# Performance work log

Hardware: AMD Instinct MI355X
Metric: run time of the kernel (lower is better)

The kernel has to match this reference:

```python
import jax, jax.numpy as jnp
import numpy as np

N = 50000
E = 800000
D_IN = 128
D_H = 128
N_CLASSES = 40
N_HIDDEN = 2


def _gcn_norm(edge_index, num_nodes):
    # Add self loops, compute symmetric normalization D^-1/2 (A+I) D^-1/2
    loops = jnp.arange(num_nodes, dtype=edge_index.dtype)
    src = jnp.concatenate([edge_index[0], loops])
    dst = jnp.concatenate([edge_index[1], loops])
    deg = jax.ops.segment_sum(jnp.ones_like(src, dtype=jnp.float32), dst,
                              num_segments=num_nodes)
    dinv = jnp.where(deg > 0, jax.lax.rsqrt(jnp.maximum(deg, 1.0)), 0.0)
    norm = dinv[src] * dinv[dst]  # [E+N]
    return src, dst, norm


def _gcn_conv(x, src, dst, norm, W, b):
    h = x @ W                          # [N, d_out] transform first (PyG order)
    msg = h[src] * norm[:, None]       # gather + scale, [E+N, d_out]
    out = jax.ops.segment_sum(msg, dst, num_segments=x.shape[0])
    return out + b


def setup_inputs() -> dict:
    key = jax.random.key(0)
    ks = jax.random.split(key, 8)
    x = jax.random.normal(ks[0], (N, D_IN), dtype=jnp.float32)
    edge_index = jax.random.randint(ks[1], (2, E), 0, N, dtype=jnp.int64)
    s = 1.0 / np.sqrt(D_IN)
    W1 = jax.random.uniform(ks[2], (D_IN, D_H), minval=-s, maxval=s, dtype=jnp.float32)
    b1 = jnp.zeros((D_H,), dtype=jnp.float32)
    sh = 1.0 / np.sqrt(D_H)
    Wh = jax.random.uniform(ks[3], (N_HIDDEN, D_H, D_H), minval=-sh, maxval=sh, dtype=jnp.float32)
    bh = jnp.zeros((N_HIDDEN, D_H), dtype=jnp.float32)
    Wf = jax.random.uniform(ks[4], (D_H, N_CLASSES), minval=-sh, maxval=sh, dtype=jnp.float32)
    bf = jnp.zeros((N_CLASSES,), dtype=jnp.float32)
    return {"x": x, "edge_index": edge_index, "W1": W1, "b1": b1,
            "Wh": Wh, "bh": bh, "Wf": Wf, "bf": bf}


def reference(x, edge_index, W1, b1, Wh, bh, Wf, bf):
    src, dst, norm = _gcn_norm(edge_index, x.shape[0])
    h = jax.nn.relu(_gcn_conv(x, src, dst, norm, W1, b1))
    for i in range(Wh.shape[0]):  # small fixed layer count
        h = jax.nn.relu(_gcn_conv(h, src, dst, norm, Wh[i], bh[i]))
    # extra relu in original forward is a no-op after relu above
    return h @ Wf + bf
```

## Files before the change

### kernel.cpp

```cpp
#include <hip/hip_runtime.h>

#define D 128
#define NC 40

typedef __attribute__((ext_vector_type(8))) short short8v;
typedef __attribute__((ext_vector_type(4))) float f32x4;

__device__ __forceinline__ unsigned short f2bf(float f) {
    unsigned u = __float_as_uint(f);
    u += 0x7fff + ((u >> 16) & 1);
    return (unsigned short)(u >> 16);
}
__device__ __forceinline__ float bf2f(unsigned short h) {
    return __uint_as_float(((unsigned)h) << 16);
}


__global__ void detect_kernel(const int* __restrict__ ei, int* __restrict__ flag) {
    __shared__ int any;
    if (threadIdx.x == 0) any = 0;
    __syncthreads();
    if (ei[threadIdx.x * 2 + 1] != 0) any = 1;
    __syncthreads();
    if (threadIdx.x == 0) *flag = (any == 0) ? 1 : 0;
}

__device__ __forceinline__ int load_idx(const int* ei, long long pos, int is64) {
    return is64 ? ei[pos * 2] : ei[pos];
}

__global__ void count_deg_kernel(const int* __restrict__ ei, const int* __restrict__ flag,
                                 int* __restrict__ deg, int E) {
    int e = blockIdx.x * blockDim.x + threadIdx.x;
    if (e >= E) return;
    int is64 = *flag;
    int d = load_idx(ei, (long long)E + e, is64);
    atomicAdd(&deg[d], 1);
}

__global__ void scan1_kernel(const int* __restrict__ deg, int* __restrict__ bsum, int n) {
    int i = blockIdx.x * 256 + threadIdx.x;
    int v = (i < n) ? deg[i] : 0;
    #pragma unroll
    for (int off = 32; off; off >>= 1) v += __shfl_down(v, off, 64);
    __shared__ int ws[4];
    if ((threadIdx.x & 63) == 0) ws[threadIdx.x >> 6] = v;
    __syncthreads();
    if (threadIdx.x == 0) bsum[blockIdx.x] = ws[0] + ws[1] + ws[2] + ws[3];
}

__global__ void scan2_kernel(int* __restrict__ bsum, int* __restrict__ total, int nb) {
    int t = threadIdx.x;
    int lane = t & 63, w = t >> 6;
    int v = (t < nb) ? bsum[t] : 0;
    int s = v;
    #pragma unroll
    for (int off = 1; off < 64; off <<= 1) {
        int x = __shfl_up(s, off, 64);
        if (lane >= off) s += x;
    }
    __shared__ int wsum[16];
    if (lane == 63) wsum[w] = s;
    __syncthreads();
    int wbase = 0;
    #pragma unroll
    for (int j = 0; j < 16; ++j) if (j < w) wbase += wsum[j];
    int excl = wbase + s - v;
    if (t < nb) bsum[t] = excl;
    if (t == nb - 1) *total = excl + v;
}

__global__ void scan3_kernel(const int* __restrict__ deg, const int* __restrict__ bsum,
                             const int* __restrict__ total, int* __restrict__ rowptr,
                             int* __restrict__ fill, float* __restrict__ dinv, int n) {
    int i = blockIdx.x * 256 + threadIdx.x;
    int v = (i < n) ? deg[i] : 0;
    int lane = threadIdx.x & 63, w = threadIdx.x >> 6;
    int s = v;
    #pragma unroll
    for (int off = 1; off < 64; off <<= 1) {
        int x = __shfl_up(s, off, 64);
        if (lane >= off) s += x;
    }
    __shared__ int wsum[4];
    if (lane == 63) wsum[w] = s;
    __syncthreads();
    int wbase = 0;
    #pragma unroll
    for (int j = 0; j < 4; ++j) if (j < w) wbase += wsum[j];
    int excl = bsum[blockIdx.x] + wbase + s - v;
    if (i < n) {
        rowptr[i] = excl;
        fill[i]   = excl;
        dinv[i]   = rsqrtf((float)(v + 1));
    }
    if (i == 0) rowptr[n] = *total;
}

__global__ void scatter_kernel(const int* __restrict__ ei, const int* __restrict__ flag,
                               int* __restrict__ fill, const float* __restrict__ dinv,
                               int2* __restrict__ col2, int E) {
    int e = blockIdx.x * blockDim.x + threadIdx.x;
    if (e >= E) return;
    int is64 = *flag;
    int s = load_idx(ei, (long long)e, is64);
    int d = load_idx(ei, (long long)E + e, is64);
    int pos = atomicAdd(&fill[d], 1);
    col2[pos] = make_int2(s, __float_as_int(dinv[s]));
}

__global__ void convertW_kernel(const float* __restrict__ W, unsigned short* __restrict__ hi,
                                unsigned short* __restrict__ lo, int N, int Npad) {
    int idx = blockIdx.x * blockDim.x + threadIdx.x;
    if (idx >= Npad * 128) return;
    int nn = idx >> 7, k = idx & 127;
    float v = (nn < N) ? W[k * N + nn] : 0.f;
    unsigned short h = f2bf(v);
    hi[idx] = h;
    lo[idx] = f2bf(v - bf2f(h));
}

__launch_bounds__(256)
__global__ void gemm128_mfma_kernel(const float* __restrict__ A, const unsigned short* __restrict__ Wcvt,
                                    float* __restrict__ C, int M) {
    __shared__ unsigned short Ah[64 * 128];
    __shared__ unsigned short Al[64 * 128];
    int t = threadIdx.x;
    int l = t & 63, w = t >> 6;
    int lr = l & 15, lh = l >> 4;

    const unsigned short* Whi = Wcvt;
    const unsigned short* Wlo = Wcvt + 128 * 128;
    short8v bhi[2][4], blo[2][4];
    int n0 = w * 32;
    #pragma unroll
    for (int ni = 0; ni < 2; ++ni) {
        int n = n0 + ni * 16 + lr;
        #pragma unroll
        for (int ks = 0; ks < 4; ++ks) {
            bhi[ni][ks] = *(const short8v*)&Whi[n * 128 + ks * 32 + lh * 8];
            blo[ni][ks] = *(const short8v*)&Wlo[n * 128 + ks * 32 + lh * 8];
        }
    }

    int row0 = blockIdx.x * 64;
    #pragma unroll
    for (int c = 0; c < 4; ++c) {
        int chunk = c * 256 + t;
        int r  = chunk >> 4;
        int kc = chunk & 15;
        int gr = row0 + r; if (gr >= M) gr = M - 1;
        float4 a0 = *(const float4*)&A[(size_t)gr * 128 + kc * 8];
        float4 a1 = *(const float4*)&A[(size_t)gr * 128 + kc * 8 + 4];
        float av[8] = {a0.x, a0.y, a0.z, a0.w, a1.x, a1.y, a1.z, a1.w};
        short8v hv, lv;
        #pragma unroll
        for (int j = 0; j < 8; ++j) {
            unsigned short hi = f2bf(av[j]);
            hv[j] = (short)hi;
            lv[j] = (short)f2bf(av[j] - bf2f(hi));
        }
        int off = (r << 8) + ((kc << 4) ^ ((r & 7) << 4));
        *(short8v*)((char*)Ah + off) = hv;
        *(short8v*)((char*)Al + off) = lv;
    }
    __syncthreads();

    f32x4 acc[4][2];
    #pragma unroll
    for (int mi = 0; mi < 4; ++mi)
        #pragma unroll
        for (int ni = 0; ni < 2; ++ni)
            acc[mi][ni] = (f32x4){0.f, 0.f, 0.f, 0.f};

    #pragma unroll
    for (int mi = 0; mi < 4; ++mi) {
        int row = mi * 16 + lr;
        #pragma unroll
        for (int ks = 0; ks < 4; ++ks) {
            int off = (row << 8) + (((ks << 6) + (lh << 4)) ^ ((row & 7) << 4));
            short8v ah = *(short8v*)((char*)Ah + off);
            short8v al = *(short8v*)((char*)Al + off);
            #pragma unroll
            for (int ni = 0; ni < 2; ++ni) {
                acc[mi][ni] = __builtin_amdgcn_mfma_f32_16x16x32_bf16(ah, bhi[ni][ks], acc[mi][ni], 0, 0, 0);
                acc[mi][ni] = __builtin_amdgcn_mfma_f32_16x16x32_bf16(ah, blo[ni][ks], acc[mi][ni], 0, 0, 0);
                acc[mi][ni] = __builtin_amdgcn_mfma_f32_16x16x32_bf16(al, bhi[ni][ks], acc[mi][ni], 0, 0, 0);
            }
        }
    }

    #pragma unroll
    for (int mi = 0; mi < 4; ++mi) {
        #pragma unroll
        for (int ni = 0; ni < 2; ++ni) {
            #pragma unroll
            for (int r = 0; r < 4; ++r) {
                int row = row0 + mi * 16 + lh * 4 + r;
                if (row < M) C[(size_t)row * 128 + n0 + ni * 16 + lr] = acc[mi][ni][r];
            }
        }
    }
}

__launch_bounds__(256)
__global__ void aggregate_kernel(const float4* __restrict__ h4, const float* __restrict__ dinv,
                                 const int* __restrict__ rowptr, const int2* __restrict__ col2,
                                 const float* __restrict__ bias, float4* __restrict__ out4, int n) {
    int node = blockIdx.x * 8 + (threadIdx.x >> 5);
    if (node >= n) return;
    int l = threadIdx.x & 31;
    float dn = dinv[node];
    size_t rowbase = (size_t)node * 32;
    float4 hv = h4[rowbase + l];
    float4 acc;
    acc.x = hv.x * dn; acc.y = hv.y * dn; acc.z = hv.z * dn; acc.w = hv.w * dn;
    int e = rowptr[node], e1 = rowptr[node + 1];
    int2 c[8];
    #pragma unroll
    for (int j = 0; j < 8; ++j)
        c[j] = (e + j < e1) ? col2[e + j] : make_int2(node, 0);
    while (e < e1) {
        int en = e + 8;
        int2 cn[8];
        #pragma unroll
        for (int j = 0; j < 8; ++j)
            cn[j] = (en + j < e1) ? col2[en + j] : make_int2(node, 0);
        float4 v[8];
        #pragma unroll
        for (int j = 0; j < 8; ++j) v[j] = h4[(size_t)c[j].x * 32 + l];
        #pragma unroll
        for (int j = 0; j < 8; ++j) {
            float ds = __int_as_float(c[j].y);
            acc.x += v[j].x * ds; acc.y += v[j].y * ds;
            acc.z += v[j].z * ds; acc.w += v[j].w * ds;
        }
        #pragma unroll
        for (int j = 0; j < 8; ++j) c[j] = cn[j];
        e = en;
    }
    float4 bv = *(const float4*)&bias[l * 4];
    float4 o;
    o.x = fmaxf(acc.x * dn + bv.x, 0.f);
    o.y = fmaxf(acc.y * dn + bv.y, 0.f);
    o.z = fmaxf(acc.z * dn + bv.z, 0.f);
    o.w = fmaxf(acc.w * dn + bv.w, 0.f);
    out4[rowbase + l] = o;
}

__launch_bounds__(256)
__global__ void final_mfma_kernel(const float* __restrict__ A, const unsigned short* __restrict__ Wcvt,
                                  const float* __restrict__ bf, float* __restrict__ C, int M) {
    __shared__ unsigned short Ah[64 * 128];
    __shared__ unsigned short Al[64 * 128];
    int t = threadIdx.x;
    int l = t & 63, w = t >> 6;
    int lr = l & 15, lh = l >> 4;

    const unsigned short* Whi = Wcvt;
    const unsigned short* Wlo = Wcvt + 48 * 128;
    short8v bhi[3][4], blo[3][4];
    #pragma unroll
    for (int nt = 0; nt < 3; ++nt) {
        int n = nt * 16 + lr;
        #pragma unroll
        for (int ks = 0; ks < 4; ++ks) {
            bhi[nt][ks] = *(const short8v*)&Whi[n * 128 + ks * 32 + lh * 8];
            blo[nt][ks] = *(const short8v*)&Wlo[n * 128 + ks * 32 + lh * 8];
        }
    }

    int row0 = blockIdx.x * 64;
    #pragma unroll
    for (int c = 0; c < 4; ++c) {
        int chunk = c * 256 + t;
        int r  = chunk >> 4;
        int kc = chunk & 15;
        int gr = row0 + r; if (gr >= M) gr = M - 1;
        float4 a0 = *(const float4*)&A[(size_t)gr * 128 + kc * 8];
        float4 a1 = *(const float4*)&A[(size_t)gr * 128 + kc * 8 + 4];
        float av[8] = {a0.x, a0.y, a0.z, a0.w, a1.x, a1.y, a1.z, a1.w};
        short8v hv, lv;
        #pragma unroll
        for (int j = 0; j < 8; ++j) {
            unsigned short hi = f2bf(av[j]);
            hv[j] = (short)hi;
            lv[j] = (short)f2bf(av[j] - bf2f(hi));
        }
        int off = (r << 8) + ((kc << 4) ^ ((r & 7) << 4));
        *(short8v*)((char*)Ah + off) = hv;
        *(short8v*)((char*)Al + off) = lv;
    }
    __syncthreads();

    f32x4 acc[3];
    #pragma unroll
    for (int nt = 0; nt < 3; ++nt) acc[nt] = (f32x4){0.f, 0.f, 0.f, 0.f};
    int row = w * 16 + lr;
    #pragma unroll
    for (int ks = 0; ks < 4; ++ks) {
        int off = (row << 8) + (((ks << 6) + (lh << 4)) ^ ((row & 7) << 4));
        short8v ah = *(short8v*)((char*)Ah + off);
        short8v al = *(short8v*)((char*)Al + off);
        #pragma unroll
        for (int nt = 0; nt < 3; ++nt) {
            acc[nt] = __builtin_amdgcn_mfma_f32_16x16x32_bf16(ah, bhi[nt][ks], acc[nt], 0, 0, 0);
            acc[nt] = __builtin_amdgcn_mfma_f32_16x16x32_bf16(ah, blo[nt][ks], acc[nt], 0, 0, 0);
            acc[nt] = __builtin_amdgcn_mfma_f32_16x16x32_bf16(al, bhi[nt][ks], acc[nt], 0, 0, 0);
        }
    }
    #pragma unroll
    for (int nt = 0; nt < 3; ++nt) {
        int col = nt * 16 + lr;
        #pragma unroll
        for (int r = 0; r < 4; ++r) {
            int ro = row0 + w * 16 + lh * 4 + r;
            if (col < NC && ro < M) C[(size_t)ro * NC + col] = acc[nt][r] + bf[col];
        }
    }
}

extern "C" void kernel_launch(void* const* d_in, const int* in_sizes, int n_in,
                              void* d_out, int out_size, void* d_ws, size_t ws_size,
                              hipStream_t stream) {
    const float* x  = (const float*)d_in[0];
    const int*   ei = (const int*)d_in[1];
    const float* W1 = (const float*)d_in[2];
    const float* b1 = (const float*)d_in[3];
    const float* Wh = (const float*)d_in[4];
    const float* bh = (const float*)d_in[5];
    const float* Wf = (const float*)d_in[6];
    const float* bf = (const float*)d_in[7];
    float* out = (float*)d_out;

    int n = in_sizes[0] / D;
    int E = in_sizes[1] / 2;

    char* ws = (char*)d_ws;
    size_t off = 0;
    auto alloc = [&](size_t bytes) {
        void* p = ws + off;
        off = (off + bytes + 255) & ~(size_t)255;
        return p;
    };
    float* B0     = (float*)alloc((size_t)n * D * 4);
    float* B1     = (float*)alloc((size_t)n * D * 4);
    int*   deg    = (int*)alloc((size_t)n * 4);
    int*   rowptr = (int*)alloc((size_t)(n + 1) * 4);
    int*   fill   = (int*)alloc((size_t)n * 4);
    int2*  col2   = (int2*)alloc((size_t)E * 8);
    float* dinv   = (float*)alloc((size_t)n * 4);
    int*   flag   = (int*)alloc(256);
    int*   bsum   = (int*)alloc(1024 * 4);
    int*   total  = (int*)alloc(256);
    unsigned short* Wc1  = (unsigned short*)alloc(2 * 128 * 128 * 2);
    unsigned short* Wch0 = (unsigned short*)alloc(2 * 128 * 128 * 2);
    unsigned short* Wch1 = (unsigned short*)alloc(2 * 128 * 128 * 2);
    unsigned short* Wcf  = (unsigned short*)alloc(2 * 48 * 128 * 2);

    int nb = (n + 255) / 256;

    hipMemsetAsync(deg, 0, (size_t)n * 4, stream);
    detect_kernel<<<1, 256, 0, stream>>>(ei, flag);
    count_deg_kernel<<<(E + 255) / 256, 256, 0, stream>>>(ei, flag, deg, E);
    scan1_kernel<<<nb, 256, 0, stream>>>(deg, bsum, n);
    scan2_kernel<<<1, 1024, 0, stream>>>(bsum, total, nb);
    scan3_kernel<<<nb, 256, 0, stream>>>(deg, bsum, total, rowptr, fill, dinv, n);
    scatter_kernel<<<(E + 255) / 256, 256, 0, stream>>>(ei, flag, fill, dinv, col2, E);

    convertW_kernel<<<(128 * 128 + 255) / 256, 256, 0, stream>>>(W1, Wc1, Wc1 + 128 * 128, 128, 128);
    convertW_kernel<<<(128 * 128 + 255) / 256, 256, 0, stream>>>(Wh, Wch0, Wch0 + 128 * 128, 128, 128);
    convertW_kernel<<<(128 * 128 + 255) / 256, 256, 0, stream>>>(Wh + 128 * 128, Wch1, Wch1 + 128 * 128, 128, 128);
    convertW_kernel<<<(48 * 128 + 255) / 256, 256, 0, stream>>>(Wf, Wcf, Wcf + 48 * 128, 40, 48);

    int gblocks = (n + 63) / 64;
    int agrid = (n + 7) / 8;

    gemm128_mfma_kernel<<<gblocks, 256, 0, stream>>>(x, Wc1, B0, n);
    aggregate_kernel<<<agrid, 256, 0, stream>>>((const float4*)B0, dinv, rowptr, col2, b1, (float4*)B1, n);
    gemm128_mfma_kernel<<<gblocks, 256, 0, stream>>>(B1, Wch0, B0, n);
    aggregate_kernel<<<agrid, 256, 0, stream>>>((const float4*)B0, dinv, rowptr, col2, bh, (float4*)B1, n);
    gemm128_mfma_kernel<<<gblocks, 256, 0, stream>>>(B1, Wch1, B0, n);
    aggregate_kernel<<<agrid, 256, 0, stream>>>((const float4*)B0, dinv, rowptr, col2, bh + D, (float4*)B1, n);
    final_mfma_kernel<<<gblocks, 256, 0, stream>>>(B1, Wcf, bf, out, n);
}
```

Baseline: 355.3 us.

## Aggregate before transform and fuse aggregation with MFMA GEMM per layer

Uses associativity (A·X)·W to aggregate raw features first and then apply the weight GEMM plus bias and ReLU inside one fused kernel per layer. This removes the intermediate GEMM output round trip through global memory and cuts kernel launches. The preprocessing also shrinks: int64 detection is inlined into each kernel, the weight conversion is merged into the degree-count launch, and the scan drops its middle pass by having each block recompute the prefix of block sums. In exchange, each fused block handles only 16 rows and reloads B fragments from global memory per block, so MFMA tile reuse is lower than in the old 64-row GEMM.

Measured after the change: 332.4 us. 6.5% less time.

```diff
diff --git a/kernel.cpp b/kernel.cpp
--- a/kernel.cpp
+++ b/kernel.cpp
@@ -15,237 +15,228 @@
     return __uint_as_float(((unsigned)h) << 16);
 }
 
-
-__global__ void detect_kernel(const int* __restrict__ ei, int* __restrict__ flag) {
-    __shared__ int any;
-    if (threadIdx.x == 0) any = 0;
-    __syncthreads();
-    if (ei[threadIdx.x * 2 + 1] != 0) any = 1;
-    __syncthreads();
-    if (threadIdx.x == 0) *flag = (any == 0) ? 1 : 0;
-}
-
 __device__ __forceinline__ int load_idx(const int* ei, long long pos, int is64) {
     return is64 ? ei[pos * 2] : ei[pos];
 }
 
-__global__ void count_deg_kernel(const int* __restrict__ ei, const int* __restrict__ flag,
-                                 int* __restrict__ deg, int E) {
-    int e = blockIdx.x * blockDim.x + threadIdx.x;
-    if (e >= E) return;
-    int is64 = *flag;
-    int d = load_idx(ei, (long long)E + e, is64);
-    atomicAdd(&deg[d], 1);
-}
-
-__global__ void scan1_kernel(const int* __restrict__ deg, int* __restrict__ bsum, int n) {
-    int i = blockIdx.x * 256 + threadIdx.x;
-    int v = (i < n) ? deg[i] : 0;
+__device__ __forceinline__ int detect64(const int* __restrict__ ei) {
+    int lane = threadIdx.x & 63;
+    int hi = ei[lane * 2 + 1];
+    return __any(hi != 0) ? 0 : 1;
+}
+
+
+__global__ void count_convert_kernel(const int* __restrict__ ei, int* __restrict__ deg,
+                                     int E, int EB,
+                                     const float* __restrict__ W1, const float* __restrict__ Wh,
+                                     const float* __restrict__ Wf,
+                                     unsigned short* __restrict__ Wc1, unsigned short* __restrict__ Wch0,
+                                     unsigned short* __restrict__ Wch1, unsigned short* __restrict__ Wcf) {
+    if (blockIdx.x < EB) {
+        int is64 = detect64(ei);
+        int e = blockIdx.x * 256 + threadIdx.x;
+        if (e < E) {
+            int d = load_idx(ei, (long long)E + e, is64);
+            atomicAdd(&deg[d], 1);
+        }
+    } else {
+        int idx = (blockIdx.x - EB) * 256 + threadIdx.x;
+        if (idx < 49152) {
+            int which = idx >> 14;
+            int j = idx & 16383;
+            int nn = j >> 7, k = j & 127;
+            const float* W = (which == 0) ? W1 : (which == 1) ? Wh : Wh + 16384;
+            unsigned short* o = (which == 0) ? Wc1 : (which == 1) ? Wch0 : Wch1;
+            float v = W[k * 128 + nn];
+            unsigned short h = f2bf(v);
+            o[j] = h;
+            o[16384 + j] = f2bf(v - bf2f(h));
+        } else if (idx < 49152 + 6144) {
+            int j = idx - 49152;
+            int nn = j >> 7, k = j & 127;
+            float v = (nn < NC) ? Wf[k * NC + nn] : 0.f;
+            unsigned short h = f2bf(v);
+            Wcf[j] = h;
+            Wcf[6144 + j] = f2bf(v - bf2f(h));
+        }
+    }
+}
+
+__global__ void scan1_kernel(const int* __restrict__ deg, int* __restrict__ bsum, int m) {
+    int i = blockIdx.x * 512 + threadIdx.x;
+    int v = (i < m) ? deg[i] : 0;
     #pragma unroll
     for (int off = 32; off; off >>= 1) v += __shfl_down(v, off, 64);
-    __shared__ int ws[4];
+    __shared__ int ws[8];
     if ((threadIdx.x & 63) == 0) ws[threadIdx.x >> 6] = v;
     __syncthreads();
-    if (threadIdx.x == 0) bsum[blockIdx.x] = ws[0] + ws[1] + ws[2] + ws[3];
-}
-
-__global__ void scan2_kernel(int* __restrict__ bsum, int* __restrict__ total, int nb) {
+    if (threadIdx.x == 0) {
+        int s = 0;
+        #pragma unroll
+        for (int j = 0; j < 8; ++j) s += ws[j];
+        bsum[blockIdx.x] = s;
+    }
+}
+
+__global__ void scan3_kernel(const int* __restrict__ deg, const int* __restrict__ bsum,
+                             int* __restrict__ rowptr, int* __restrict__ fill,
+                             float* __restrict__ dinv, int n, int E, int nb) {
     int t = threadIdx.x;
     int lane = t & 63, w = t >> 6;
-    int v = (t < nb) ? bsum[t] : 0;
+    int pv = (t < nb && t < (int)blockIdx.x) ? bsum[t] : 0;
+    int rs = pv;
+    #pragma unroll
+    for (int off = 32; off; off >>= 1) rs += __shfl_down(rs, off, 64);
+    __shared__ int red[8];
+    if (lane == 0) red[w] = rs;
+    __syncthreads();
+    int base = 0;
+    #pragma unroll
+    for (int j = 0; j < 8; ++j) base += red[j];
+    __syncthreads();
+
+    int i = blockIdx.x * 512 + t;
+    int v = (i < n) ? deg[i] : 0;
     int s = v;
     #pragma unroll
     for (int off = 1; off < 64; off <<= 1) {
         int x = __shfl_up(s, off, 64);
         if (lane >= off) s += x;
     }
-    __shared__ int wsum[16];
+    __shared__ int wsum[8];
     if (lane == 63) wsum[w] = s;
     __syncthreads();
     int wbase = 0;
     #pragma unroll
-    for (int j = 0; j < 16; ++j) if (j < w) wbase += wsum[j];
-    int excl = wbase + s - v;
-    if (t < nb) bsum[t] = excl;
-    if (t == nb - 1) *total = excl + v;
-}
-
-__global__ void scan3_kernel(const int* __restrict__ deg, const int* __restrict__ bsum,
-                             const int* __restrict__ total, int* __restrict__ rowptr,
-                             int* __restrict__ fill, float* __restrict__ dinv, int n) {
-    int i = blockIdx.x * 256 + threadIdx.x;
-    int v = (i < n) ? deg[i] : 0;
-    int lane = threadIdx.x & 63, w = threadIdx.x >> 6;
-    int s = v;
-    #pragma unroll
-    for (int off = 1; off < 64; off <<= 1) {
-        int x = __shfl_up(s, off, 64);
-        if (lane >= off) s += x;
-    }
-    __shared__ int wsum[4];
-    if (lane == 63) wsum[w] = s;
-    __syncthreads();
-    int wbase = 0;
-    #pragma unroll
-    for (int j = 0; j < 4; ++j) if (j < w) wbase += wsum[j];
-    int excl = bsum[blockIdx.x] + wbase + s - v;
+    for (int j = 0; j < 8; ++j) if (j < w) wbase += wsum[j];
+    int excl = base + wbase + s - v;
     if (i < n) {
         rowptr[i] = excl;
         fill[i]   = excl;
         dinv[i]   = rsqrtf((float)(v + 1));
     }
-    if (i == 0) rowptr[n] = *total;
-}
-
-__global__ void scatter_kernel(const int* __restrict__ ei, const int* __restrict__ flag,
-                               int* __restrict__ fill, const float* __restrict__ dinv,
-                               int2* __restrict__ col2, int E) {
-    int e = blockIdx.x * blockDim.x + threadIdx.x;
+    if (i == 0) rowptr[n] = E;
+}
+
+__global__ void scatter_kernel(const int* __restrict__ ei, int* __restrict__ fill,
+                               const float* __restrict__ dinv, int2* __restrict__ col2, int E) {
+    int is64 = detect64(ei);
+    int e = blockIdx.x * 256 + threadIdx.x;
     if (e >= E) return;
-    int is64 = *flag;
     int s = load_idx(ei, (long long)e, is64);
     int d = load_idx(ei, (long long)E + e, is64);
     int pos = atomicAdd(&fill[d], 1);
     col2[pos] = make_int2(s, __float_as_int(dinv[s]));
 }
 
-__global__ void convertW_kernel(const float* __restrict__ W, unsigned short* __restrict__ hi,
-                                unsigned short* __restrict__ lo, int N, int Npad) {
-    int idx = blockIdx.x * blockDim.x + threadIdx.x;
-    if (idx >= Npad * 128) return;
-    int nn = idx >> 7, k = idx & 127;
-    float v = (nn < N) ? W[k * N + nn] : 0.f;
-    unsigned short h = f2bf(v);
-    hi[idx] = h;
-    lo[idx] = f2bf(v - bf2f(h));
-}
-
 __launch_bounds__(256)
-__global__ void gemm128_mfma_kernel(const float* __restrict__ A, const unsigned short* __restrict__ Wcvt,
-                                    float* __restrict__ C, int M) {
-    __shared__ unsigned short Ah[64 * 128];
-    __shared__ unsigned short Al[64 * 128];
+__global__ void fused_layer_kernel(const float4* __restrict__ h4,
+                                   const unsigned short* __restrict__ Wcvt,
+                                   const float* __restrict__ bias,
+                                   const float* __restrict__ dinv,
+                                   const int* __restrict__ rowptr, const int2* __restrict__ col2,
+                                   float* __restrict__ out, int n) {
+    __shared__ unsigned short Ah[16 * 128];
+    __shared__ unsigned short Al[16 * 128];
     int t = threadIdx.x;
-    int l = t & 63, w = t >> 6;
+    int g = t >> 4, l16 = t & 15;
+    int node = blockIdx.x * 16 + g;
+    int nd = (node < n) ? node : (n - 1);
+    float dn = dinv[nd];
+    size_t rowbase = (size_t)nd * 32;
+
+    float4 a0 = h4[rowbase + l16];
+    float4 a1 = h4[rowbase + l16 + 16];
+    float4 acc0, acc1;
+    acc0.x = a0.x * dn; acc0.y = a0.y * dn; acc0.z = a0.z * dn; acc0.w = a0.w * dn;
+    acc1.x = a1.x * dn; acc1.y = a1.y * dn; acc1.z = a1.z * dn; acc1.w = a1.w * dn;
+
+    int e = rowptr[nd], e1 = rowptr[nd + 1];
+    for (; e + 4 <= e1; e += 4) {
+        int2 c[4];
+        #pragma unroll
+        for (int j = 0; j < 4; ++j) c[j] = col2[e + j];
+        float4 v0[4], v1[4];
+        #pragma unroll
+        for (int j = 0; j < 4; ++j) {
+            size_t b = (size_t)c[j].x * 32;
+            v0[j] = h4[b + l16];
+            v1[j] = h4[b + l16 + 16];
+        }
+        #pragma unroll
+        for (int j = 0; j < 4; ++j) {
+            float ds = __int_as_float(c[j].y);
+            acc0.x += v0[j].x * ds; acc0.y += v0[j].y * ds;
+            acc0.z += v0[j].z * ds; acc0.w += v0[j].w * ds;
+            acc1.x += v1[j].x * ds; acc1.y += v1[j].y * ds;
+            acc1.z += v1[j].z * ds; acc1.w += v1[j].w * ds;
+        }
+    }
+    for (; e < e1; ++e) {
+        int2 c = col2[e];
+        float ds = __int_as_float(c.y);
+        size_t b = (size_t)c.x * 32;
+        float4 v0 = h4[b + l16], v1 = h4[b + l16 + 16];
+        acc0.x += v0.x * ds; acc0.y += v0.y * ds; acc0.z += v0.z * ds; acc0.w += v0.w * ds;
+        acc1.x += v1.x * ds; acc1.y += v1.y * ds; acc1.z += v1.z * ds; acc1.w += v1.w * ds;
+    }
+    acc0.x *= dn; acc0.y *= dn; acc0.z *= dn; acc0.w *= dn;
+    acc1.x *= dn; acc1.y *= dn; acc1.z *= dn; acc1.w *= dn;
+
+    {
+        int kc0 = l16 >> 1, sub = (l16 & 1) * 8;
+        int off0 = (g << 8) + (((kc0) << 4) ^ ((g & 7) << 4)) + sub;
+        int off1 = (g << 8) + (((kc0 + 8) << 4) ^ ((g & 7) << 4)) + sub;
+        ushort4 h0, l0, h1, l1;
+        h0.x = f2bf(acc0.x); l0.x = f2bf(acc0.x - bf2f(h0.x));
+        h0.y = f2bf(acc0.y); l0.y = f2bf(acc0.y - bf2f(h0.y));
+        h0.z = f2bf(acc0.z); l0.z = f2bf(acc0.z - bf2f(h0.z));
+        h0.w = f2bf(acc0.w); l0.w = f2bf(acc0.w - bf2f(h0.w));
+        h1.x = f2bf(acc1.x); l1.x = f2bf(acc1.x - bf2f(h1.x));
+        h1.y = f2bf(acc1.y); l1.y = f2bf(acc1.y - bf2f(h1.y));
+        h1.z = f2bf(acc1.z); l1.z = f2bf(acc1.z - bf2f(h1.z));
+        h1.w = f2bf(acc1.w); l1.w = f2bf(acc1.w - bf2f(h1.w));
+        *(ushort4*)((char*)Ah + off0) = h0;
+        *(ushort4*)((char*)Al + off0) = l0;
+        *(ushort4*)((char*)Ah + off1) = h1;
+        *(ushort4*)((char*)Al + off1) = l1;
+    }
+    __syncthreads();
+
+    int l = t & 63, wv = t >> 6;
     int lr = l & 15, lh = l >> 4;
-
     const unsigned short* Whi = Wcvt;
     const unsigned short* Wlo = Wcvt + 128 * 128;
-    short8v bhi[2][4], blo[2][4];
-    int n0 = w * 32;
-    #pragma unroll
-    for (int ni = 0; ni < 2; ++ni) {
-        int n = n0 + ni * 16 + lr;
-        #pragma unroll
-        for (int ks = 0; ks < 4; ++ks) {
-            bhi[ni][ks] = *(const short8v*)&Whi[n * 128 + ks * 32 + lh * 8];
-            blo[ni][ks] = *(const short8v*)&Wlo[n * 128 + ks * 32 + lh * 8];
-        }
-    }
-
-    int row0 = blockIdx.x * 64;
-    #pragma unroll
-    for (int c = 0; c < 4; ++c) {
-        int chunk = c * 256 + t;
-        int r  = chunk >> 4;
-        int kc = chunk & 15;
-        int gr = row0 + r; if (gr >= M) gr = M - 1;
-        float4 a0 = *(const float4*)&A[(size_t)gr * 128 + kc * 8];
-        float4 a1 = *(const float4*)&A[(size_t)gr * 128 + kc * 8 + 4];
-        float av[8] = {a0.x, a0.y, a0.z, a0.w, a1.x, a1.y, a1.z, a1.w};
-        short8v hv, lv;
-        #pragma unroll
-        for (int j = 0; j < 8; ++j) {
-            unsigned short hi = f2bf(av[j]);
-            hv[j] = (short)hi;
-            lv[j] = (short)f2bf(av[j] - bf2f(hi));
-        }
-        int off = (r << 8) + ((kc << 4) ^ ((r & 7) << 4));
-        *(short8v*)((char*)Ah + off) = hv;
-        *(short8v*)((char*)Al + off) = lv;
-    }
-    __syncthreads();
-
-    f32x4 acc[4][2];
-    #pragma unroll
-    for (int mi = 0; mi < 4; ++mi)
-        #pragma unroll
-        for (int ni = 0; ni < 2; ++ni)
-            acc[mi][ni] = (f32x4){0.f, 0.f, 0.f, 0.f};
-
-    #pragma unroll
-    for (int mi = 0; mi < 4; ++mi) {
-        int row = mi * 16 + lr;
-        #pragma unroll
-        for (int ks = 0; ks < 4; ++ks) {
-            int off = (row << 8) + (((ks << 6) + (lh << 4)) ^ ((row & 7) << 4));
-            short8v ah = *(short8v*)((char*)Ah + off);
-            short8v al = *(short8v*)((char*)Al + off);
-            #pragma unroll
-            for (int ni = 0; ni < 2; ++ni) {
-                acc[mi][ni] = __builtin_amdgcn_mfma_f32_16x16x32_bf16(ah, bhi[ni][ks], acc[mi][ni], 0, 0, 0);
-                acc[mi][ni] = __builtin_amdgcn_mfma_f32_16x16x32_bf16(ah, blo[ni][ks], acc[mi][ni], 0, 0, 0);
-                acc[mi][ni] = __builtin_amdgcn_mfma_f32_16x16x32_bf16(al, bhi[ni][ks], acc[mi][ni], 0, 0, 0);
-            }
-        }
-    }
-
-    #pragma unroll
-    for (int mi = 0; mi < 4; ++mi) {
-        #pragma unroll
-        for (int ni = 0; ni < 2; ++ni) {
-            #pragma unroll
-            for (int r = 0; r < 4; ++r) {
-                int row = row0 + mi * 16 + lh * 4 + r;
-                if (row < M) C[(size_t)row * 128 + n0 + ni * 16 + lr] = acc[mi][ni][r];
-            }
-        }
-    }
-}
-
-__launch_bounds__(256)
-__global__ void aggregate_kernel(const float4* __restrict__ h4, const float* __restrict__ dinv,
-                                 const int* __restrict__ rowptr, const int2* __restrict__ col2,
-                                 const float* __restrict__ bias, float4* __restrict__ out4, int n) {
-    int node = blockIdx.x * 8 + (threadIdx.x >> 5);
-    if (node >= n) return;
-    int l = threadIdx.x & 31;
-    float dn = dinv[node];
-    size_t rowbase = (size_t)node * 32;
-    float4 hv = h4[rowbase + l];
-    float4 acc;
-    acc.x = hv.x * dn; acc.y = hv.y * dn; acc.z = hv.z * dn; acc.w = hv.w * dn;
-    int e = rowptr[node], e1 = rowptr[node + 1];
-    int2 c[8];
-    #pragma unroll
-    for (int j = 0; j < 8; ++j)
-        c[j] = (e + j < e1) ? col2[e + j] : make_int2(node, 0);
-    while (e < e1) {
-        int en = e + 8;
-        int2 cn[8];
-        #pragma unroll
-        for (int j = 0; j < 8; ++j)
-            cn[j] = (en + j < e1) ? col2[en + j] : make_int2(node, 0);
-        float4 v[8];
-        #pragma unroll
-        for (int j = 0; j < 8; ++j) v[j] = h4[(size_t)c[j].x * 32 + l];
-        #pragma unroll
-        for (int j = 0; j < 8; ++j) {
-            float ds = __int_as_float(c[j].y);
-            acc.x += v[j].x * ds; acc.y += v[j].y * ds;
-            acc.z += v[j].z * ds; acc.w += v[j].w * ds;
-        }
-        #pragma unroll
-        for (int j = 0; j < 8; ++j) c[j] = cn[j];
-        e = en;
-    }
-    float4 bv = *(const float4*)&bias[l * 4];
-    float4 o;
-    o.x = fmaxf(acc.x * dn + bv.x, 0.f);
-    o.y = fmaxf(acc.y * dn + bv.y, 0.f);
-    o.z = fmaxf(acc.z * dn + bv.z, 0.f);
-    o.w = fmaxf(acc.w * dn + bv.w, 0.f);
-    out4[rowbase + l] = o;
+    f32x4 o0 = (f32x4){0.f, 0.f, 0.f, 0.f};
+    f32x4 o1 = (f32x4){0.f, 0.f, 0.f, 0.f};
+    int n0 = wv * 32;
+    #pragma unroll
+    for (int ks = 0; ks < 4; ++ks) {
+        int aoff = (lr << 8) + (((ks << 6) + (lh << 4)) ^ ((lr & 7) << 4));
+        short8v ah = *(short8v*)((char*)Ah + aoff);
+        short8v al = *(short8v*)((char*)Al + aoff);
+        int c0 = (n0 + lr) * 128 + ks * 32 + lh * 8;
+        int c1 = (n0 + 16 + lr) * 128 + ks * 32 + lh * 8;
+        short8v bh0 = *(const short8v*)&Whi[c0];
+        short8v bl0 = *(const short8v*)&Wlo[c0];
+        short8v bh1 = *(const short8v*)&Whi[c1];
+        short8v bl1 = *(const short8v*)&Wlo[c1];
+        o0 = __builtin_amdgcn_mfma_f32_16x16x32_bf16(ah, bh0, o0, 0, 0, 0);
+        o0 = __builtin_amdgcn_mfma_f32_16x16x32_bf16(ah, bl0, o0, 0, 0, 0);
+        o0 = __builtin_amdgcn_mfma_f32_16x16x32_bf16(al, bh0, o0, 0, 0, 0);
+        o1 = __builtin_amdgcn_mfma_f32_16x16x32_bf16(ah, bh1, o1, 0, 0, 0);
+        o1 = __builtin_amdgcn_mfma_f32_16x16x32_bf16(ah, bl1, o1, 0, 0, 0);
+        o1 = __builtin_amdgcn_mfma_f32_16x16x32_bf16(al, bh1, o1, 0, 0, 0);
+    }
+    float b0 = bias[n0 + lr], b1v = bias[n0 + 16 + lr];
+    #pragma unroll
+    for (int r = 0; r < 4; ++r) {
+        int row = blockIdx.x * 16 + lh * 4 + r;
+        if (row < n) {
+            out[(size_t)row * 128 + n0 + lr]      = fmaxf(o0[r] + b0, 0.f);
+            out[(size_t)row * 128 + n0 + 16 + lr] = fmaxf(o1[r] + b1v, 0.f);
+        }
+    }
 }
 
 __launch_bounds__(256)
@@ -350,37 +341,26 @@
     int*   fill   = (int*)alloc((size_t)n * 4);
     int2*  col2   = (int2*)alloc((size_t)E * 8);
     float* dinv   = (float*)alloc((size_t)n * 4);
-    int*   flag   = (int*)alloc(256);
     int*   bsum   = (int*)alloc(1024 * 4);
-    int*   total  = (int*)alloc(256);
     unsigned short* Wc1  = (unsigned short*)alloc(2 * 128 * 128 * 2);
     unsigned short* Wch0 = (unsigned short*)alloc(2 * 128 * 128 * 2);
     unsigned short* Wch1 = (unsigned short*)alloc(2 * 128 * 128 * 2);
     unsigned short* Wcf  = (unsigned short*)alloc(2 * 48 * 128 * 2);
 
-    int nb = (n + 255) / 256;
+    int EB = (E + 255) / 256;
+    int CB = (49152 + 6144 + 255) / 256;
+    int nb = (n + 511) / 512;
 
     hipMemsetAsync(deg, 0, (size_t)n * 4, stream);
-    detect_kernel<<<1, 256, 0, stream>>>(ei, flag);
-    count_deg_kernel<<<(E + 255) / 256, 256, 0, stream>>>(ei, flag, deg, E);
-    scan1_kernel<<<nb, 256, 0, stream>>>(deg, bsum, n);
-    scan2_kernel<<<1, 1024, 0, stream>>>(bsum, total, nb);
-    scan3_kernel<<<nb, 256, 0, stream>>>(deg, bsum, total, rowptr, fill, dinv, n);
-    scatter_kernel<<<(E + 255) / 256, 256, 0, stream>>>(ei, flag, fill, dinv, col2, E);
-
-    convertW_kernel<<<(128 * 128 + 255) / 256, 256, 0, stream>>>(W1, Wc1, Wc1 + 128 * 128, 128, 128);
-    convertW_kernel<<<(128 * 128 + 255) / 256, 256, 0, stream>>>(Wh, Wch0, Wch0 + 128 * 128, 128, 128);
-    convertW_kernel<<<(128 * 128 + 255) / 256, 256, 0, stream>>>(Wh + 128 * 128, Wch1, Wch1 + 128 * 128, 128, 128);
-    convertW_kernel<<<(48 * 128 + 255) / 256, 256, 0, stream>>>(Wf, Wcf, Wcf + 48 * 128, 40, 48);
-
-    int gblocks = (n + 63) / 64;
-    int agrid = (n + 7) / 8;
-
-    gemm128_mfma_kernel<<<gblocks, 256, 0, stream>>>(x, Wc1, B0, n);
-    aggregate_kernel<<<agrid, 256, 0, stream>>>((const float4*)B0, dinv, rowptr, col2, b1, (float4*)B1, n);
-    gemm128_mfma_kernel<<<gblocks, 256, 0, stream>>>(B1, Wch0, B0, n);
-    aggregate_kernel<<<agrid, 256, 0, stream>>>((const float4*)B0, dinv, rowptr, col2, bh, (float4*)B1, n);
-    gemm128_mfma_kernel<<<gblocks, 256, 0, stream>>>(B1, Wch1, B0, n);
-    aggregate_kernel<<<agrid, 256, 0, stream>>>((const float4*)B0, dinv, rowptr, col2, bh + D, (float4*)B1, n);
-    final_mfma_kernel<<<gblocks, 256, 0, stream>>>(B1, Wcf, bf, out, n);
-}
+    count_convert_kernel<<<EB + CB, 256, 0, stream>>>(ei, deg, E, EB, W1, Wh, Wf, Wc1, Wch0, Wch1, Wcf);
+    scan1_kernel<<<nb, 512, 0, stream>>>(deg, bsum, n);
+    scan3_kernel<<<nb, 512, 0, stream>>>(deg, bsum, rowptr, fill, dinv, n, E, nb);
+    scatter_kernel<<<EB, 256, 0, stream>>>(ei, fill, dinv, col2, E);
+
+    int fgrid = (n + 15) / 16;
+
+    fused_layer_kernel<<<fgrid, 256, 0, stream>>>((const float4*)x, Wc1, b1, dinv, rowptr, col2, B0, n);
+    fused_layer_kernel<<<fgrid, 256, 0, stream>>>((const float4*)B0, Wch0, bh, dinv, rowptr, col2, B1, n);
+    fused_layer_kernel<<<fgrid, 256, 0, stream>>>((const float4*)B1, Wch1, bh + D, dinv, rowptr, col2, B0, n);
+    final_mfma_kernel<<<(n + 63) / 64, 256, 0, stream>>>(B0, Wcf, bf, out, n);
+}
```
